# Performance work log

Measured on AMD Instinct MI355X. Metric: run time of the kernel, lower is better.

Reference implementation:

```python
import jax, jax.numpy as jnp
import numpy as np

IN_CHANNELS = 64
OUT_CHANNELS = 64
MODES = 64


def setup_inputs() -> dict:
    key = jax.random.key(0)
    kq, kk, kv = jax.random.split(key, 3)
    B, L, E, H = 16, 2048, 64, 8
    S = 2048
    q = jax.random.normal(kq, (B, L, E, H), dtype=jnp.float32)
    k = jax.random.normal(kk, (B, S, E, H), dtype=jnp.float32)
    v = jax.random.normal(kv, (B, S, E, H), dtype=jnp.float32)
    return {"q": q, "k": k, "v": v}


def reference(q, k, v):
    # q: [B,L,E,H], k/v: [B,S,E,H]. v is unused (matches the source module).
    B, L, E, H = q.shape
    S = k.shape[1]
    Mq = min(L // 2, MODES)
    Mkv = min(S // 2, MODES)

    xq = jnp.transpose(q, (0, 3, 2, 1))  # [B,H,E,L]
    xk = jnp.transpose(k, (0, 3, 2, 1))  # [B,H,E,S]

    # rFFT along time, keep lowest Mq/Mkv modes (index_q/index_kv are range(...))
    xq_ft = jnp.fft.rfft(xq, axis=-1)[..., :Mq]    # [B,H,E,Mq] complex64
    xk_ft = jnp.fft.rfft(xk, axis=-1)[..., :Mkv]   # [B,H,E,Mkv]

    # compl_mul1d is a plain complex multiply inside einsum (no conjugate)
    xqk_ft = jnp.einsum('bhex,bhey->bhxy', xq_ft, xk_ft)  # [B,H,Mq,Mkv]

    # tanh applied separately to real and imaginary parts
    xqk_ft = jax.lax.complex(jnp.tanh(xqk_ft.real), jnp.tanh(xqk_ft.imag))

    xqkv_ft = jnp.einsum('bhxy,bhey->bhex', xqk_ft, xk_ft)  # [B,H,E,Mq]

    # scatter selected modes into zero spectrum, then inverse FFT
    out_ft = jnp.zeros((B, H, E, L // 2 + 1), dtype=jnp.complex64)
    out_ft = out_ft.at[..., :Mq].set(xqkv_ft)
    scale = jnp.float32(IN_CHANNELS * OUT_CHANNELS)
    out = jnp.fft.irfft(out_ft / scale, n=L, axis=-1)  # [B,H,E,L] real
    return jnp.transpose(out, (0, 3, 1, 2))  # [B,L,H,E]
```

## Files before the change

kernel.cpp:

```cpp
#include <hip/hip_runtime.h>
#include <math.h>

typedef __attribute__((ext_vector_type(8))) short short8v;
typedef __attribute__((ext_vector_type(16))) float f32x16;

#define BF_U 0
#define BI_U 262144
#define XP_F 270336
#define YT_U 17317888

__device__ inline unsigned short bf16_rne(float x) {
    unsigned int u = __float_as_uint(x);
    u += 0x7FFFu + ((u >> 16) & 1u);
    return (unsigned short)(u >> 16);
}
__device__ inline float bf16_f(unsigned short h) {
    return __uint_as_float(((unsigned int)h) << 16);
}

__global__ __launch_bounds__(256) void basis_kernel(float* __restrict__ w) {
    int idx = blockIdx.x * 256 + threadIdx.x;
    const float th = 0.0030679615757712823f;
    unsigned short* bw = (unsigned short*)w;
    if (idx < 65536) {
        int t = idx >> 6, m = idx & 63;
        int j = (m * t) & 2047;
        float s, c; sincosf(th * (float)j, &s, &c);
        float ns = -s;
        int cc = t >> 4, kh = (t >> 3) & 1, e = t & 7;
        int base = BF_U + cc * 4096 + kh * 512 + m * 8 + e;
        unsigned short chv = bf16_rne(c), shv = bf16_rne(ns);
        bw[base]        = chv;
        bw[base + 1024] = bf16_rne(c - bf16_f(chv));
        bw[base + 2048] = shv;
        bw[base + 3072] = bf16_rne(ns - bf16_f(shv));
    }
    if (idx < 69632) {
        int m = idx / 1088, t = idx - m * 1088;
        int j = (m * t) & 2047;
        float s, c; sincosf(th * (float)j, &s, &c);
        int slab = m >> 4, kh = (m >> 3) & 1, e = m & 7;
        int base = BI_U + (slab * 8 + kh) * 8704 + t * 8 + e;
        unsigned short chv = bf16_rne(c), shv = bf16_rne(s);
        bw[base]         = chv;
        bw[base + 17408] = bf16_rne(c - bf16_f(chv));
        bw[base + 34816] = shv;
        bw[base + 52224] = bf16_rne(s - bf16_f(shv));
    }
}

__global__ __launch_bounds__(256, 4) void fdft_kernel(const float* __restrict__ q,
                                                      const float* __restrict__ k,
                                                      float* __restrict__ ws) {
    const int chtile = blockIdx.x;
    const int b      = blockIdx.y;
    const int zz     = blockIdx.z >> 1;
    const int mgrp   = blockIdx.z & 1;
    const int part   = zz & 3;
    const float* __restrict__ src = (zz >> 2) ? k : q;
    const unsigned short* __restrict__ basisF = (const unsigned short*)ws + BF_U;
    float* __restrict__ xp = ws + XP_F + (size_t)(zz * 16 + b) * 65536;

    __shared__ __align__(16) unsigned short lds[2][8192];

    const int tid  = threadIdx.x;
    const int lane = tid & 63;
    const int wc   = tid >> 6;
    const int ml   = lane & 31;
    const int khl  = lane >> 5;

    const int chl = tid & 127;
    const int kh  = tid >> 7;
    const float* __restrict__ ap = src + (size_t)b * 2048 * 512 + chtile * 128 + chl;

    f32x16 accR, accI;
#pragma unroll
    for (int i = 0; i < 16; ++i) { accR[i] = 0.f; accI[i] = 0.f; }

    float av[8], pv[8];

    auto LOAD = [&](int s) {
        const int t0 = part * 256 + s * 16 + kh * 8;
#pragma unroll
        for (int e = 0; e < 8; ++e) {
            int t = t0 + e;
            int pr = (t == 0) ? 1024 : 2048 - t;
            av[e] = ap[(size_t)t * 512];
            pv[e] = ap[(size_t)pr * 512];
        }
    };
    auto WRITE = [&](int bf) {
        unsigned short* D = &lds[bf][0];
        short8v xu, xl, xv, xw;
#pragma unroll
        for (int e = 0; e < 8; ++e) {
            float u = av[e] + pv[e], v = av[e] - pv[e];
            unsigned short uh = bf16_rne(u); unsigned short vh = bf16_rne(v);
            xu[e] = (short)uh; xl[e] = (short)bf16_rne(u - bf16_f(uh));
            xv[e] = (short)vh; xw[e] = (short)bf16_rne(v - bf16_f(vh));
        }
        const int doff = kh * 1024 + chl * 8;
        *(short8v*)(D + doff)        = xu;
        *(short8v*)(D + doff + 2048) = xl;
        *(short8v*)(D + doff + 4096) = xv;
        *(short8v*)(D + doff + 6144) = xw;
    };
    auto COMP = [&](int bf, int s) {
        const unsigned short* bb = basisF + (part * 16 + s) * 4096
                                 + khl * 512 + (mgrp * 32 + ml) * 8;
        short8v cH = *(const short8v*)(bb);
        short8v cL = *(const short8v*)(bb + 1024);
        short8v sH = *(const short8v*)(bb + 2048);
        short8v sL = *(const short8v*)(bb + 3072);
        const unsigned short* L = &lds[bf][0];
        const int b0 = khl * 1024 + (wc * 32 + ml) * 8;
        short8v uH = *(const short8v*)(L + b0);
        short8v uL = *(const short8v*)(L + b0 + 2048);
        short8v vH = *(const short8v*)(L + b0 + 4096);
        short8v vL = *(const short8v*)(L + b0 + 6144);
        accR = __builtin_amdgcn_mfma_f32_32x32x16_bf16(cH, uH, accR, 0, 0, 0);
        accR = __builtin_amdgcn_mfma_f32_32x32x16_bf16(cH, uL, accR, 0, 0, 0);
        accR = __builtin_amdgcn_mfma_f32_32x32x16_bf16(cL, uH, accR, 0, 0, 0);
        accI = __builtin_amdgcn_mfma_f32_32x32x16_bf16(sH, vH, accI, 0, 0, 0);
        accI = __builtin_amdgcn_mfma_f32_32x32x16_bf16(sH, vL, accI, 0, 0, 0);
        accI = __builtin_amdgcn_mfma_f32_32x32x16_bf16(sL, vH, accI, 0, 0, 0);
    };

    LOAD(0); WRITE(0); __syncthreads();
    for (int s = 0; s < 16; ++s) {
        if (s < 15) LOAD(s + 1);
        COMP(s & 1, s);
        if (s < 15) { WRITE((s + 1) & 1); __syncthreads(); }
    }

    if (part == 0) {
        float a0 = src[(size_t)b * 2048 * 512 + (size_t)1024 * 512
                       + chtile * 128 + wc * 32 + ml];
#pragma unroll
        for (int reg = 1; reg < 16; reg += 2) accR[reg] -= 2.f * a0;
    }

    float* LF = (float*)(&lds[0][0]);
#pragma unroll 1
    for (int pass = 0; pass < 2; ++pass) {
        __syncthreads();
#pragma unroll
        for (int reg = 0; reg < 16; ++reg) {
            const int mL = (reg & 3) + 8 * (reg >> 2) + 4 * khl;
            LF[mL * 129 + wc * 32 + ml] = pass ? accI[reg] : accR[reg];
        }
        __syncthreads();
#pragma unroll
        for (int u8 = 0; u8 < 4; ++u8) {
            int unit = tid + u8 * 256;
            int e4 = unit & 3, h = (unit >> 2) & 7, mL = unit >> 5;
            float4 val;
            val.x = LF[mL * 129 + ((e4 * 4 + 0) * 8 + h)];
            val.y = LF[mL * 129 + ((e4 * 4 + 1) * 8 + h)];
            val.z = LF[mL * 129 + ((e4 * 4 + 2) * 8 + h)];
            val.w = LF[mL * 129 + ((e4 * 4 + 3) * 8 + h)];
            *(float4*)&xp[pass * 32768 + (h * 64 + mgrp * 32 + mL) * 64
                          + chtile * 16 + e4 * 4] = val;
        }
    }
}

__global__ __launch_bounds__(128) void mid_kernel(float* __restrict__ ws) {
    const int h = blockIdx.x, b = blockIdx.y, xh = blockIdx.z;
    unsigned short* __restrict__ YTb = (unsigned short*)ws + YT_U + (size_t)b * 131072;

    __shared__ float Qs[2][32][64];
    __shared__ float Ksw[2][64][64];

    const int tid = threadIdx.x;
    for (int slot = tid; slot < 1024; slot += 128) {
        int p = slot >> 9, ml = (slot >> 4) & 31, c4 = slot & 15;
        int off = ((p * 8 + h) * 64 + xh * 32 + ml) * 64 + c4 * 4;
        float4 acc = make_float4(0.f, 0.f, 0.f, 0.f);
#pragma unroll
        for (int part = 0; part < 4; ++part) {
            const float4 v = *(const float4*)(ws + XP_F + (size_t)(part * 16 + b) * 65536 + off);
            acc.x += v.x; acc.y += v.y; acc.z += v.z; acc.w += v.w;
        }
        *(float4*)(&Qs[p][ml][c4 * 4]) = acc;
    }
    for (int slot = tid; slot < 2048; slot += 128) {
        int p = slot >> 10, ml = (slot >> 4) & 63, c4 = slot & 15;
        int off = ((p * 8 + h) * 64 + ml) * 64 + c4 * 4;
        float4 acc = make_float4(0.f, 0.f, 0.f, 0.f);
#pragma unroll
        for (int part = 0; part < 4; ++part) {
            const float4 v = *(const float4*)(ws + XP_F + (size_t)((4 + part) * 16 + b) * 65536 + off);
            acc.x += v.x; acc.y += v.y; acc.z += v.z; acc.w += v.w;
        }
        Ksw[p][ml][(c4 * 4 + 0) ^ ml] = acc.x;
        Ksw[p][ml][(c4 * 4 + 1) ^ ml] = acc.y;
        Ksw[p][ml][(c4 * 4 + 2) ^ ml] = acc.z;
        Ksw[p][ml][(c4 * 4 + 3) ^ ml] = acc.w;
    }
    __syncthreads();

    const int lane = tid & 63;
    const int wid  = tid >> 6;
    const int xb   = wid * 16;

    float sr[16], si[16];
#pragma unroll
    for (int i = 0; i < 16; ++i) { sr[i] = 0.f; si[i] = 0.f; }
    const int y = lane;
    for (int e = 0; e < 64; ++e) {
        float kr = Ksw[0][y][e ^ y];
        float ki = Ksw[1][y][e ^ y];
#pragma unroll
        for (int i = 0; i < 16; ++i) {
            float qr = Qs[0][xb + i][e];
            float qi = Qs[1][xb + i][e];
            sr[i] += qr * kr; sr[i] -= qi * ki;
            si[i] += qr * ki; si[i] += qi * kr;
        }
    }
    float tr[16], ti[16];
#pragma unroll
    for (int i = 0; i < 16; ++i) { tr[i] = tanhf(sr[i]); ti[i] = tanhf(si[i]); }
    __syncthreads();
#pragma unroll
    for (int i = 0; i < 16; ++i) {
        Qs[0][xb + i][y] = tr[i];
        Qs[1][xb + i][y] = ti[i];
    }
    __syncthreads();

    float vr[16], vi[16];
#pragma unroll
    for (int i = 0; i < 16; ++i) { vr[i] = 0.f; vi[i] = 0.f; }
    const int e = lane;
    for (int yy = 0; yy < 64; ++yy) {
        float kr = Ksw[0][yy][e ^ yy];
        float ki = Ksw[1][yy][e ^ yy];
#pragma unroll
        for (int i = 0; i < 16; ++i) {
            float trr = Qs[0][xb + i][yy];
            float tii = Qs[1][xb + i][yy];
            vr[i] += trr * kr; vr[i] -= tii * ki;
            vi[i] += trr * ki; vi[i] += tii * kr;
        }
    }
#pragma unroll
    for (int i = 0; i < 16; ++i) {
        int x = xh * 32 + xb + i;
        float f = (x == 0 ? 1.0f : 2.0f) * (1.0f / (2048.0f * 4096.0f));
        float yr = f * vr[i];
        float yi = -f * vi[i];
        int off = (h * 64 + e) * 64 + x;
        unsigned short rH = bf16_rne(yr), iH = bf16_rne(yi);
        YTb[off]         = rH;
        YTb[32768 + off] = bf16_rne(yr - bf16_f(rH));
        YTb[65536 + off] = iH;
        YTb[98304 + off] = bf16_rne(yi - bf16_f(iH));
    }
}

__global__ __launch_bounds__(256, 3) void idft_kernel(const float* __restrict__ ws,
                                                      float* __restrict__ out) {
    const int tt0    = blockIdx.x * 64;
    const int chtile = blockIdx.y;
    const int b      = blockIdx.z;
    const unsigned short* __restrict__ basisI = (const unsigned short*)ws + BI_U;
    const unsigned short* __restrict__ YTb = (const unsigned short*)ws + YT_U + (size_t)b * 131072;

    __shared__ __align__(16) unsigned short ldsY[2][12288];

    const int tid  = threadIdx.x;
    const int lane = tid & 63;
    const int wv   = tid >> 6;
    const int wt   = wv >> 1, wcc = wv & 1;
    const int ml   = lane & 31;
    const int khl  = lane >> 5;

    f32x16 accP0, accP1, accQ0, accQ1;
#pragma unroll
    for (int i = 0; i < 16; ++i) { accP0[i] = 0.f; accP1[i] = 0.f; accQ0[i] = 0.f; accQ1[i] = 0.f; }

    const int tblA = tid >> 7;
    const int chlA = tid & 127;
    short8v sA0, sA1, sB0, sB1;

    auto LOAD = [&](int s) {
        const unsigned short* gA = YTb + tblA * 32768 + (chtile * 128 + chlA) * 64 + s * 16;
        const unsigned short* gB = gA + 2 * 32768;
        sA0 = *(const short8v*)(gA);
        sA1 = *(const short8v*)(gA + 8);
        sB0 = *(const short8v*)(gB);
        sB1 = *(const short8v*)(gB + 8);
    };
    auto WRITE = [&](int bf) {
        unsigned short* D = &ldsY[bf][0];
        const int offA = tblA * 3072 + chlA * 24;
        *(short8v*)(D + offA)            = sA0;
        *(short8v*)(D + offA + 8)        = sA1;
        *(short8v*)(D + offA + 2 * 3072)     = sB0;
        *(short8v*)(D + offA + 2 * 3072 + 8) = sB1;
    };
    auto COMP = [&](int bf, int s) {
        const unsigned short* bb = basisI + (s * 8 + khl) * 8704 + (tt0 + wt * 32 + ml) * 8;
        short8v cH = *(const short8v*)(bb);
        short8v cL = *(const short8v*)(bb + 17408);
        short8v sH = *(const short8v*)(bb + 34816);
        short8v sL = *(const short8v*)(bb + 52224);
        const unsigned short* L = &ldsY[bf][0];
        const int b0 = (wcc * 64 + ml) * 24 + khl * 8;
        short8v yrH0 = *(const short8v*)(L + b0);
        short8v yrL0 = *(const short8v*)(L + 3072 + b0);
        short8v yiH0 = *(const short8v*)(L + 6144 + b0);
        short8v yiL0 = *(const short8v*)(L + 9216 + b0);
        const int b1 = b0 + 32 * 24;
        short8v yrH1 = *(const short8v*)(L + b1);
        short8v yrL1 = *(const short8v*)(L + 3072 + b1);
        short8v yiH1 = *(const short8v*)(L + 6144 + b1);
        short8v yiL1 = *(const short8v*)(L + 9216 + b1);
        accP0 = __builtin_amdgcn_mfma_f32_32x32x16_bf16(cH, yrH0, accP0, 0, 0, 0);
        accP0 = __builtin_amdgcn_mfma_f32_32x32x16_bf16(cH, yrL0, accP0, 0, 0, 0);
        accP0 = __builtin_amdgcn_mfma_f32_32x32x16_bf16(cL, yrH0, accP0, 0, 0, 0);
        accQ0 = __builtin_amdgcn_mfma_f32_32x32x16_bf16(sH, yiH0, accQ0, 0, 0, 0);
        accQ0 = __builtin_amdgcn_mfma_f32_32x32x16_bf16(sH, yiL0, accQ0, 0, 0, 0);
        accQ0 = __builtin_amdgcn_mfma_f32_32x32x16_bf16(sL, yiH0, accQ0, 0, 0, 0);
        accP1 = __builtin_amdgcn_mfma_f32_32x32x16_bf16(cH, yrH1, accP1, 0, 0, 0);
        accP1 = __builtin_amdgcn_mfma_f32_32x32x16_bf16(cH, yrL1, accP1, 0, 0, 0);
        accP1 = __builtin_amdgcn_mfma_f32_32x32x16_bf16(cL, yrH1, accP1, 0, 0, 0);
        accQ1 = __builtin_amdgcn_mfma_f32_32x32x16_bf16(sH, yiH1, accQ1, 0, 0, 0);
        accQ1 = __builtin_amdgcn_mfma_f32_32x32x16_bf16(sH, yiL1, accQ1, 0, 0, 0);
        accQ1 = __builtin_amdgcn_mfma_f32_32x32x16_bf16(sL, yiH1, accQ1, 0, 0, 0);
    };

    LOAD(0); WRITE(0); __syncthreads();
    for (int s = 0; s < 4; ++s) {
        if (s < 3) LOAD(s + 1);
        COMP(s & 1, s);
        if (s < 3) { WRITE((s + 1) & 1); __syncthreads(); }
    }

    float* __restrict__ ob = out + (size_t)b * 2048 * 512;
#pragma unroll
    for (int reg = 0; reg < 16; ++reg) {
        const int tL = wt * 32 + (reg & 3) + 8 * (reg >> 2) + 4 * khl;
        const int t  = tt0 + tL;
        const int ch0 = chtile * 128 + wcc * 64 + ml;
        float p0 = accP0[reg], q0 = accQ0[reg];
        float p1 = accP1[reg], q1 = accQ1[reg];
        if (t <= 1024) {
            ob[(size_t)t * 512 + ch0]      = p0 + q0;
            ob[(size_t)t * 512 + ch0 + 32] = p1 + q1;
        }
        if (t >= 1 && t <= 1023) {
            ob[(size_t)(2048 - t) * 512 + ch0]      = p0 - q0;
            ob[(size_t)(2048 - t) * 512 + ch0 + 32] = p1 - q1;
        }
    }
}

extern "C" void kernel_launch(void* const* d_in, const int* in_sizes, int n_in,
                              void* d_out, int out_size, void* d_ws, size_t ws_size,
                              hipStream_t stream) {
    const float* q = (const float*)d_in[0];
    const float* k = (const float*)d_in[1];
    float* ws = (float*)d_ws;
    float* out = (float*)d_out;

    hipLaunchKernelGGL(basis_kernel, dim3(272), dim3(256), 0, stream, ws);
    hipLaunchKernelGGL(fdft_kernel, dim3(4, 16, 16), dim3(256), 0, stream, q, k, ws);
    hipLaunchKernelGGL(mid_kernel, dim3(8, 16, 2), dim3(128), 0, stream, ws);
    hipLaunchKernelGGL(idft_kernel, dim3(17, 4, 16), dim3(256), 0, stream, ws, out);
}
```

Baseline: 107.9 us.

## Retile forward DFT so each block covers all modes over a narrower channel tile

The forward DFT kernel now gives each block all 64 modes split across 2x2 waves for a 64-channel tile, where before each block held 32 modes for 128 channels. This removes the duplicate global loads of q/k that the two mode-group blocks used to make. Loads are double-buffered with two register sets so two steps are in flight, and the LDS transpose uses an XOR swizzle in place of padding. The grid keeps the same block count, but each block's input reads are halved, and the epilogue stores shorter contiguous runs into the workspace.

New measurement: 106.6 us. Within noise of the previous version (-1.1%).

```diff
diff --git a/kernel.cpp b/kernel.cpp
--- a/kernel.cpp
+++ b/kernel.cpp
@@ -1,6 +1,7 @@
 #include <hip/hip_runtime.h>
 #include <math.h>
 
+typedef __attribute__((ext_vector_type(4))) short short4v;
 typedef __attribute__((ext_vector_type(8))) short short8v;
 typedef __attribute__((ext_vector_type(16))) float f32x16;
 
@@ -54,88 +55,102 @@
                                                       float* __restrict__ ws) {
     const int chtile = blockIdx.x;
     const int b      = blockIdx.y;
-    const int zz     = blockIdx.z >> 1;
-    const int mgrp   = blockIdx.z & 1;
+    const int zz     = blockIdx.z;
     const int part   = zz & 3;
     const float* __restrict__ src = (zz >> 2) ? k : q;
     const unsigned short* __restrict__ basisF = (const unsigned short*)ws + BF_U;
     float* __restrict__ xp = ws + XP_F + (size_t)(zz * 16 + b) * 65536;
 
-    __shared__ __align__(16) unsigned short lds[2][8192];
+    __shared__ __align__(16) unsigned short lds[2][4096];
 
     const int tid  = threadIdx.x;
     const int lane = tid & 63;
-    const int wc   = tid >> 6;
+    const int wv   = tid >> 6;
+    const int wm   = wv >> 1, wc = wv & 1;
     const int ml   = lane & 31;
     const int khl  = lane >> 5;
 
-    const int chl = tid & 127;
-    const int kh  = tid >> 7;
-    const float* __restrict__ ap = src + (size_t)b * 2048 * 512 + chtile * 128 + chl;
+    const int chl  = tid & 63;
+    const int kh   = (tid >> 6) & 1;
+    const int half = tid >> 7;
+    const float* __restrict__ ap = src + (size_t)b * 2048 * 512 + chtile * 64 + chl;
 
     f32x16 accR, accI;
 #pragma unroll
     for (int i = 0; i < 16; ++i) { accR[i] = 0.f; accI[i] = 0.f; }
 
-    float av[8], pv[8];
-
-    auto LOAD = [&](int s) {
-        const int t0 = part * 256 + s * 16 + kh * 8;
-#pragma unroll
-        for (int e = 0; e < 8; ++e) {
-            int t = t0 + e;
-            int pr = (t == 0) ? 1024 : 2048 - t;
-            av[e] = ap[(size_t)t * 512];
-            pv[e] = ap[(size_t)pr * 512];
-        }
-    };
-    auto WRITE = [&](int bf) {
-        unsigned short* D = &lds[bf][0];
-        short8v xu, xl, xv, xw;
-#pragma unroll
-        for (int e = 0; e < 8; ++e) {
-            float u = av[e] + pv[e], v = av[e] - pv[e];
-            unsigned short uh = bf16_rne(u); unsigned short vh = bf16_rne(v);
-            xu[e] = (short)uh; xl[e] = (short)bf16_rne(u - bf16_f(uh));
-            xv[e] = (short)vh; xw[e] = (short)bf16_rne(v - bf16_f(vh));
-        }
-        const int doff = kh * 1024 + chl * 8;
-        *(short8v*)(D + doff)        = xu;
-        *(short8v*)(D + doff + 2048) = xl;
-        *(short8v*)(D + doff + 4096) = xv;
-        *(short8v*)(D + doff + 6144) = xw;
-    };
-    auto COMP = [&](int bf, int s) {
-        const unsigned short* bb = basisF + (part * 16 + s) * 4096
-                                 + khl * 512 + (mgrp * 32 + ml) * 8;
-        short8v cH = *(const short8v*)(bb);
-        short8v cL = *(const short8v*)(bb + 1024);
-        short8v sH = *(const short8v*)(bb + 2048);
-        short8v sL = *(const short8v*)(bb + 3072);
-        const unsigned short* L = &lds[bf][0];
-        const int b0 = khl * 1024 + (wc * 32 + ml) * 8;
-        short8v uH = *(const short8v*)(L + b0);
-        short8v uL = *(const short8v*)(L + b0 + 2048);
-        short8v vH = *(const short8v*)(L + b0 + 4096);
-        short8v vL = *(const short8v*)(L + b0 + 6144);
-        accR = __builtin_amdgcn_mfma_f32_32x32x16_bf16(cH, uH, accR, 0, 0, 0);
-        accR = __builtin_amdgcn_mfma_f32_32x32x16_bf16(cH, uL, accR, 0, 0, 0);
-        accR = __builtin_amdgcn_mfma_f32_32x32x16_bf16(cL, uH, accR, 0, 0, 0);
-        accI = __builtin_amdgcn_mfma_f32_32x32x16_bf16(sH, vH, accI, 0, 0, 0);
-        accI = __builtin_amdgcn_mfma_f32_32x32x16_bf16(sH, vL, accI, 0, 0, 0);
-        accI = __builtin_amdgcn_mfma_f32_32x32x16_bf16(sL, vH, accI, 0, 0, 0);
-    };
-
-    LOAD(0); WRITE(0); __syncthreads();
-    for (int s = 0; s < 16; ++s) {
-        if (s < 15) LOAD(s + 1);
-        COMP(s & 1, s);
-        if (s < 15) { WRITE((s + 1) & 1); __syncthreads(); }
+    float av0[4], pv0[4], av1[4], pv1[4];
+
+#define FDFT_LOAD(S, AV, PV)                                              \
+    {                                                                     \
+        const int t0 = part * 256 + (S) * 16 + kh * 8 + half * 4;         \
+        _Pragma("unroll")                                                 \
+        for (int e = 0; e < 4; ++e) {                                     \
+            int t = t0 + e;                                               \
+            int pr = (t == 0) ? 1024 : 2048 - t;                          \
+            AV[e] = ap[(size_t)t * 512];                                  \
+            PV[e] = ap[(size_t)pr * 512];                                 \
+        }                                                                 \
+    }
+
+#define FDFT_WRITE(BF, AV, PV)                                            \
+    {                                                                     \
+        unsigned short* D = &lds[BF][0];                                  \
+        short4v xu, xl, xv, xw;                                           \
+        _Pragma("unroll")                                                 \
+        for (int e = 0; e < 4; ++e) {                                     \
+            float u = AV[e] + PV[e], v = AV[e] - PV[e];                   \
+            unsigned short uh = bf16_rne(u), vh = bf16_rne(v);            \
+            xu[e] = (short)uh; xl[e] = (short)bf16_rne(u - bf16_f(uh));   \
+            xv[e] = (short)vh; xw[e] = (short)bf16_rne(v - bf16_f(vh));   \
+        }                                                                 \
+        const int off = kh * 512 + chl * 8 + half * 4;                    \
+        *(short4v*)(D + off)        = xu;                                 \
+        *(short4v*)(D + off + 1024) = xl;                                 \
+        *(short4v*)(D + off + 2048) = xv;                                 \
+        *(short4v*)(D + off + 3072) = xw;                                 \
+    }
+
+#define FDFT_COMP(BF, S)                                                  \
+    {                                                                     \
+        const unsigned short* bb = basisF + (size_t)(part * 16 + (S)) * 4096 \
+                                 + khl * 512 + (wm * 32 + ml) * 8;        \
+        short8v cH = *(const short8v*)(bb);                               \
+        short8v cL = *(const short8v*)(bb + 1024);                        \
+        short8v sH = *(const short8v*)(bb + 2048);                        \
+        short8v sL = *(const short8v*)(bb + 3072);                        \
+        const unsigned short* L = &lds[BF][0];                            \
+        const int b0 = khl * 512 + (wc * 32 + ml) * 8;                    \
+        short8v uH = *(const short8v*)(L + b0);                           \
+        short8v uL = *(const short8v*)(L + b0 + 1024);                    \
+        short8v vH = *(const short8v*)(L + b0 + 2048);                    \
+        short8v vL = *(const short8v*)(L + b0 + 3072);                    \
+        accR = __builtin_amdgcn_mfma_f32_32x32x16_bf16(cH, uH, accR, 0, 0, 0); \
+        accR = __builtin_amdgcn_mfma_f32_32x32x16_bf16(cH, uL, accR, 0, 0, 0); \
+        accR = __builtin_amdgcn_mfma_f32_32x32x16_bf16(cL, uH, accR, 0, 0, 0); \
+        accI = __builtin_amdgcn_mfma_f32_32x32x16_bf16(sH, vH, accI, 0, 0, 0); \
+        accI = __builtin_amdgcn_mfma_f32_32x32x16_bf16(sH, vL, accI, 0, 0, 0); \
+        accI = __builtin_amdgcn_mfma_f32_32x32x16_bf16(sL, vH, accI, 0, 0, 0); \
+    }
+
+    FDFT_LOAD(0, av0, pv0);
+    FDFT_LOAD(1, av1, pv1);
+    FDFT_WRITE(0, av0, pv0);
+    __syncthreads();
+
+    for (int s = 0; s < 16; s += 2) {
+        if (s + 2 < 16) FDFT_LOAD(s + 2, av0, pv0);
+        FDFT_COMP(0, s);
+        FDFT_WRITE(1, av1, pv1);
+        __syncthreads();
+        if (s + 3 < 16) FDFT_LOAD(s + 3, av1, pv1);
+        FDFT_COMP(1, s + 1);
+        if (s + 2 < 16) { FDFT_WRITE(0, av0, pv0); __syncthreads(); }
     }
 
     if (part == 0) {
         float a0 = src[(size_t)b * 2048 * 512 + (size_t)1024 * 512
-                       + chtile * 128 + wc * 32 + ml];
+                       + chtile * 64 + wc * 32 + ml];
 #pragma unroll
         for (int reg = 1; reg < 16; reg += 2) accR[reg] -= 2.f * a0;
     }
@@ -146,23 +161,27 @@
         __syncthreads();
 #pragma unroll
         for (int reg = 0; reg < 16; ++reg) {
-            const int mL = (reg & 3) + 8 * (reg >> 2) + 4 * khl;
-            LF[mL * 129 + wc * 32 + ml] = pass ? accI[reg] : accR[reg];
+            const int m = wm * 32 + (reg & 3) + 8 * (reg >> 2) + 4 * khl;
+            const int chL = wc * 32 + ml;
+            LF[m * 64 + (chL ^ ((m & 7) << 3))] = pass ? accI[reg] : accR[reg];
         }
         __syncthreads();
 #pragma unroll
         for (int u8 = 0; u8 < 4; ++u8) {
             int unit = tid + u8 * 256;
-            int e4 = unit & 3, h = (unit >> 2) & 7, mL = unit >> 5;
+            int h = unit & 7, eh = (unit >> 3) & 1, m = unit >> 4;
             float4 val;
-            val.x = LF[mL * 129 + ((e4 * 4 + 0) * 8 + h)];
-            val.y = LF[mL * 129 + ((e4 * 4 + 1) * 8 + h)];
-            val.z = LF[mL * 129 + ((e4 * 4 + 2) * 8 + h)];
-            val.w = LF[mL * 129 + ((e4 * 4 + 3) * 8 + h)];
-            *(float4*)&xp[pass * 32768 + (h * 64 + mgrp * 32 + mL) * 64
-                          + chtile * 16 + e4 * 4] = val;
-        }
-    }
+#pragma unroll
+            for (int j = 0; j < 4; ++j) {
+                int chL = (eh * 4 + j) * 8 + h;
+                ((float*)&val)[j] = LF[m * 64 + (chL ^ ((m & 7) << 3))];
+            }
+            *(float4*)&xp[pass * 32768 + (h * 64 + m) * 64 + chtile * 8 + eh * 4] = val;
+        }
+    }
+#undef FDFT_LOAD
+#undef FDFT_WRITE
+#undef FDFT_COMP
 }
 
 __global__ __launch_bounds__(128) void mid_kernel(float* __restrict__ ws) {
@@ -367,7 +386,7 @@
     float* out = (float*)d_out;
 
     hipLaunchKernelGGL(basis_kernel, dim3(272), dim3(256), 0, stream, ws);
-    hipLaunchKernelGGL(fdft_kernel, dim3(4, 16, 16), dim3(256), 0, stream, q, k, ws);
+    hipLaunchKernelGGL(fdft_kernel, dim3(8, 16, 8), dim3(256), 0, stream, q, k, ws);
     hipLaunchKernelGGL(mid_kernel, dim3(8, 16, 2), dim3(128), 0, stream, ws);
     hipLaunchKernelGGL(idft_kernel, dim3(17, 4, 16), dim3(256), 0, stream, ws, out);
 }
```

## Replace folded LDS-staged forward DFT with direct full-length register-fed MFMA DFT

Applied to the files above, without the earlier changes.

The forward DFT kernel drops the t/2048-t symmetric folding and the double-buffered LDS staging. Each wave now loads raw input samples straight into registers, splits them into bf16 hi/lo, and multiplies against a full 2048-point basis. Each block now covers all 64 modes, so every input element is read once instead of once per mode group plus its mirrored pair. This removes the per-step barriers and LDS traffic, and the output transpose gets an XOR swizzle. In exchange it doubles the MFMA work and the basis table size, since the even/odd folding is gone.

Result: slower. 120.3 us (+11.5%).

```diff
diff --git a/kernel.cpp b/kernel.cpp
--- a/kernel.cpp
+++ b/kernel.cpp
@@ -5,9 +5,9 @@
 typedef __attribute__((ext_vector_type(16))) float f32x16;
 
 #define BF_U 0
-#define BI_U 262144
-#define XP_F 270336
-#define YT_U 17317888
+#define BI_U 524288
+#define XP_F 401408
+#define YT_U 17580032
 
 __device__ inline unsigned short bf16_rne(float x) {
     unsigned int u = __float_as_uint(x);
@@ -22,7 +22,7 @@
     int idx = blockIdx.x * 256 + threadIdx.x;
     const float th = 0.0030679615757712823f;
     unsigned short* bw = (unsigned short*)w;
-    if (idx < 65536) {
+    if (idx < 131072) {
         int t = idx >> 6, m = idx & 63;
         int j = (m * t) & 2047;
         float s, c; sincosf(th * (float)j, &s, &c);
@@ -54,113 +54,76 @@
                                                       float* __restrict__ ws) {
     const int chtile = blockIdx.x;
     const int b      = blockIdx.y;
-    const int zz     = blockIdx.z >> 1;
-    const int mgrp   = blockIdx.z & 1;
+    const int zz     = blockIdx.z;
     const int part   = zz & 3;
     const float* __restrict__ src = (zz >> 2) ? k : q;
     const unsigned short* __restrict__ basisF = (const unsigned short*)ws + BF_U;
     float* __restrict__ xp = ws + XP_F + (size_t)(zz * 16 + b) * 65536;
 
-    __shared__ __align__(16) unsigned short lds[2][8192];
+    __shared__ __align__(16) float LF[4096];
 
     const int tid  = threadIdx.x;
     const int lane = tid & 63;
-    const int wc   = tid >> 6;
+    const int wv   = tid >> 6;
+    const int wm   = wv >> 1, wc = wv & 1;
     const int ml   = lane & 31;
     const int khl  = lane >> 5;
 
-    const int chl = tid & 127;
-    const int kh  = tid >> 7;
-    const float* __restrict__ ap = src + (size_t)b * 2048 * 512 + chtile * 128 + chl;
+    const int ch = chtile * 64 + wc * 32 + ml;
+    const float* __restrict__ ap = src + (size_t)b * 2048 * 512 + ch;
 
     f32x16 accR, accI;
 #pragma unroll
     for (int i = 0; i < 16; ++i) { accR[i] = 0.f; accI[i] = 0.f; }
 
-    float av[8], pv[8];
-
-    auto LOAD = [&](int s) {
-        const int t0 = part * 256 + s * 16 + kh * 8;
+#pragma unroll 2
+    for (int s = 0; s < 32; ++s) {
+        const int t0 = part * 512 + s * 16 + khl * 8;
+        float a[8];
+#pragma unroll
+        for (int e = 0; e < 8; ++e) a[e] = ap[(size_t)(t0 + e) * 512];
+        short8v uH, uL;
 #pragma unroll
         for (int e = 0; e < 8; ++e) {
-            int t = t0 + e;
-            int pr = (t == 0) ? 1024 : 2048 - t;
-            av[e] = ap[(size_t)t * 512];
-            pv[e] = ap[(size_t)pr * 512];
-        }
-    };
-    auto WRITE = [&](int bf) {
-        unsigned short* D = &lds[bf][0];
-        short8v xu, xl, xv, xw;
-#pragma unroll
-        for (int e = 0; e < 8; ++e) {
-            float u = av[e] + pv[e], v = av[e] - pv[e];
-            unsigned short uh = bf16_rne(u); unsigned short vh = bf16_rne(v);
-            xu[e] = (short)uh; xl[e] = (short)bf16_rne(u - bf16_f(uh));
-            xv[e] = (short)vh; xw[e] = (short)bf16_rne(v - bf16_f(vh));
-        }
-        const int doff = kh * 1024 + chl * 8;
-        *(short8v*)(D + doff)        = xu;
-        *(short8v*)(D + doff + 2048) = xl;
-        *(short8v*)(D + doff + 4096) = xv;
-        *(short8v*)(D + doff + 6144) = xw;
-    };
-    auto COMP = [&](int bf, int s) {
-        const unsigned short* bb = basisF + (part * 16 + s) * 4096
-                                 + khl * 512 + (mgrp * 32 + ml) * 8;
+            unsigned short hi = bf16_rne(a[e]);
+            uH[e] = (short)hi;
+            uL[e] = (short)bf16_rne(a[e] - bf16_f(hi));
+        }
+        const unsigned short* bb = basisF + (size_t)(part * 32 + s) * 4096
+                                 + khl * 512 + (wm * 32 + ml) * 8;
         short8v cH = *(const short8v*)(bb);
         short8v cL = *(const short8v*)(bb + 1024);
         short8v sH = *(const short8v*)(bb + 2048);
         short8v sL = *(const short8v*)(bb + 3072);
-        const unsigned short* L = &lds[bf][0];
-        const int b0 = khl * 1024 + (wc * 32 + ml) * 8;
-        short8v uH = *(const short8v*)(L + b0);
-        short8v uL = *(const short8v*)(L + b0 + 2048);
-        short8v vH = *(const short8v*)(L + b0 + 4096);
-        short8v vL = *(const short8v*)(L + b0 + 6144);
         accR = __builtin_amdgcn_mfma_f32_32x32x16_bf16(cH, uH, accR, 0, 0, 0);
         accR = __builtin_amdgcn_mfma_f32_32x32x16_bf16(cH, uL, accR, 0, 0, 0);
         accR = __builtin_amdgcn_mfma_f32_32x32x16_bf16(cL, uH, accR, 0, 0, 0);
-        accI = __builtin_amdgcn_mfma_f32_32x32x16_bf16(sH, vH, accI, 0, 0, 0);
-        accI = __builtin_amdgcn_mfma_f32_32x32x16_bf16(sH, vL, accI, 0, 0, 0);
-        accI = __builtin_amdgcn_mfma_f32_32x32x16_bf16(sL, vH, accI, 0, 0, 0);
-    };
-
-    LOAD(0); WRITE(0); __syncthreads();
-    for (int s = 0; s < 16; ++s) {
-        if (s < 15) LOAD(s + 1);
-        COMP(s & 1, s);
-        if (s < 15) { WRITE((s + 1) & 1); __syncthreads(); }
-    }
-
-    if (part == 0) {
-        float a0 = src[(size_t)b * 2048 * 512 + (size_t)1024 * 512
-                       + chtile * 128 + wc * 32 + ml];
-#pragma unroll
-        for (int reg = 1; reg < 16; reg += 2) accR[reg] -= 2.f * a0;
-    }
-
-    float* LF = (float*)(&lds[0][0]);
+        accI = __builtin_amdgcn_mfma_f32_32x32x16_bf16(sH, uH, accI, 0, 0, 0);
+        accI = __builtin_amdgcn_mfma_f32_32x32x16_bf16(sH, uL, accI, 0, 0, 0);
+        accI = __builtin_amdgcn_mfma_f32_32x32x16_bf16(sL, uH, accI, 0, 0, 0);
+    }
+
 #pragma unroll 1
     for (int pass = 0; pass < 2; ++pass) {
         __syncthreads();
 #pragma unroll
         for (int reg = 0; reg < 16; ++reg) {
-            const int mL = (reg & 3) + 8 * (reg >> 2) + 4 * khl;
-            LF[mL * 129 + wc * 32 + ml] = pass ? accI[reg] : accR[reg];
+            const int m = wm * 32 + (reg & 3) + 8 * (reg >> 2) + 4 * khl;
+            const int chL = wc * 32 + ml;
+            LF[m * 64 + (chL ^ ((m & 7) << 3))] = pass ? accI[reg] : accR[reg];
         }
         __syncthreads();
 #pragma unroll
         for (int u8 = 0; u8 < 4; ++u8) {
             int unit = tid + u8 * 256;
-            int e4 = unit & 3, h = (unit >> 2) & 7, mL = unit >> 5;
+            int h = unit & 7, eh = (unit >> 3) & 1, m = unit >> 4;
             float4 val;
-            val.x = LF[mL * 129 + ((e4 * 4 + 0) * 8 + h)];
-            val.y = LF[mL * 129 + ((e4 * 4 + 1) * 8 + h)];
-            val.z = LF[mL * 129 + ((e4 * 4 + 2) * 8 + h)];
-            val.w = LF[mL * 129 + ((e4 * 4 + 3) * 8 + h)];
-            *(float4*)&xp[pass * 32768 + (h * 64 + mgrp * 32 + mL) * 64
-                          + chtile * 16 + e4 * 4] = val;
+#pragma unroll
+            for (int j = 0; j < 4; ++j) {
+                int chL = (eh * 4 + j) * 8 + h;
+                ((float*)&val)[j] = LF[m * 64 + (chL ^ ((m & 7) << 3))];
+            }
+            *(float4*)&xp[pass * 32768 + (h * 64 + m) * 64 + chtile * 8 + eh * 4] = val;
         }
     }
 }
@@ -366,8 +329,8 @@
     float* ws = (float*)d_ws;
     float* out = (float*)d_out;
 
-    hipLaunchKernelGGL(basis_kernel, dim3(272), dim3(256), 0, stream, ws);
-    hipLaunchKernelGGL(fdft_kernel, dim3(4, 16, 16), dim3(256), 0, stream, q, k, ws);
+    hipLaunchKernelGGL(basis_kernel, dim3(512), dim3(256), 0, stream, ws);
+    hipLaunchKernelGGL(fdft_kernel, dim3(8, 16, 8), dim3(256), 0, stream, q, k, ws);
     hipLaunchKernelGGL(mid_kernel, dim3(8, 16, 2), dim3(128), 0, stream, ws);
     hipLaunchKernelGGL(idft_kernel, dim3(17, 4, 16), dim3(256), 0, stream, ws, out);
 }
```
